# Kernel optimization log

Hardware: AMD Instinct MI355X
Metric: run time of the kernel (lower is better)

Reference implementation:

```python
import itertools
import jax, jax.numpy as jnp
import numpy as np

H, W, DIM, NH, WS = 64, 64, 384, 12, 7
HD = DIM // NH            # head dim = key_dim (attn_ratio=1)
N = WS * WS               # tokens per window
SCALE = HD ** -0.5
EPS = 1e-5
BATCH = 4
HID = int(DIM * 4.0)


def _bias_idxs():
    points = list(itertools.product(range(WS), range(WS)))
    offsets, idxs = {}, []
    for p1 in points:
        for p2 in points:
            off = (abs(p1[0] - p2[0]), abs(p1[1] - p2[1]))
            if off not in offsets:
                offsets[off] = len(offsets)
            idxs.append(offsets[off])
    return np.asarray(idxs, dtype=np.int32).reshape(N, N)

BIAS_IDXS = _bias_idxs()              # [N, N] static
NUM_OFFSETS = int(BIAS_IDXS.max()) + 1  # 49 for a 7x7 window


def setup_inputs() -> dict:
    key = jax.random.key(0)
    ks = jax.random.split(key, 10)
    rn = lambda k, shp, s=0.02: jax.random.normal(k, shp, jnp.float32) * s
    return {
        "x": jax.random.normal(ks[0], (BATCH, H * W, DIM), jnp.float32),
        "ln1_g": jnp.ones((DIM,), jnp.float32),
        "ln1_b": jnp.zeros((DIM,), jnp.float32),
        "qkv_w": rn(ks[1], (DIM, 3 * DIM)),
        "qkv_b": jnp.zeros((3 * DIM,), jnp.float32),
        "proj_w": rn(ks[2], (DIM, DIM)),
        "proj_b": jnp.zeros((DIM,), jnp.float32),
        "attn_bias": rn(ks[3], (NH, NUM_OFFSETS), 0.1),
        "conv_w": rn(ks[4], (DIM, 1, 3, 3), 0.1),  # depthwise OIHW
        "bn_g": jnp.ones((DIM,), jnp.float32),
        "bn_b": jnp.zeros((DIM,), jnp.float32),
        "bn_mean": rn(ks[5], (DIM,), 0.05),
        "bn_var": jax.random.uniform(ks[6], (DIM,), jnp.float32, 0.5, 1.5),
        "ln2_g": jnp.ones((DIM,), jnp.float32),
        "ln2_b": jnp.zeros((DIM,), jnp.float32),
        "fc1_w": rn(ks[7], (DIM, HID)),
        "fc1_b": jnp.zeros((HID,), jnp.float32),
        "fc2_w": rn(ks[8], (HID, DIM)),
        "fc2_b": jnp.zeros((DIM,), jnp.float32),
    }


def _ln(x, g, b):
    m = x.mean(-1, keepdims=True)
    v = jnp.var(x, axis=-1, keepdims=True)
    return (x - m) * jax.lax.rsqrt(v + EPS) * g + b


def reference(x, ln1_g, ln1_b, qkv_w, qkv_b, proj_w, proj_b, attn_bias,
              conv_w, bn_g, bn_b, bn_mean, bn_var, ln2_g, ln2_b,
              fc1_w, fc1_b, fc2_w, fc2_b):
    b, hw, c = x.shape
    res = x
    # --- window partition with padding ---
    pad_b = (-H) % WS
    pad_r = (-W) % WS
    pH, pW = H + pad_b, W + pad_r
    nH, nW = pH // WS, pW // WS
    xw = x.reshape(b, H, W, c)
    xw = jnp.pad(xw, ((0, 0), (0, pad_b), (0, pad_r), (0, 0)))
    xw = xw.reshape(b, nH, WS, nW, WS, c).transpose(0, 1, 3, 2, 4, 5)
    xw = xw.reshape(b * nH * nW, N, c)  # [Bw, N, C]
    # --- attention (pre-LN, relative position bias) ---
    xn = _ln(xw, ln1_g, ln1_b)
    qkv = (xn @ qkv_w + qkv_b).reshape(-1, N, NH, 3 * HD)
    q, k, v = jnp.split(qkv, [HD, 2 * HD], axis=-1)  # each [Bw, N, NH, HD]
    bias = attn_bias[:, BIAS_IDXS]                    # [NH, N, N]
    scores = jnp.einsum('bnhd,bmhd->bhnm', q, k) * SCALE + bias
    a = jax.nn.softmax(scores, axis=-1)
    o = jnp.einsum('bhnm,bmhd->bnhd', a, v).reshape(-1, N, NH * HD)
    xw = o @ proj_w + proj_b
    # --- window reverse + unpad ---
    xw = xw.reshape(b, nH, nW, WS, WS, c).transpose(0, 1, 3, 2, 4, 5)
    xw = xw.reshape(b, pH, pW, c)[:, :H, :W].reshape(b, hw, c)
    x = res + xw
    # --- depthwise 3x3 conv + BatchNorm (eval) ---
    xc = x.transpose(0, 2, 1).reshape(b, c, H, W)
    xc = jax.lax.conv_general_dilated(
        xc, conv_w, (1, 1), ((1, 1), (1, 1)),
        feature_group_count=c,
        dimension_numbers=('NCHW', 'OIHW', 'NCHW'))
    xc = (xc - bn_mean[:, None, None]) * jax.lax.rsqrt(bn_var[:, None, None] + EPS) \
         * bn_g[:, None, None] + bn_b[:, None, None]
    x = xc.reshape(b, c, hw).transpose(0, 2, 1)
    # --- MLP (pre-LN, GELU) with residual ---
    h1 = jax.nn.gelu(_ln(x, ln2_g, ln2_b) @ fc1_w + fc1_b, approximate=False)
    return x + (h1 @ fc2_w + fc2_b)
```

## Files before the change

kernel.cpp:

```cpp
#include <hip/hip_runtime.h>
#include <cstdint>


typedef __bf16 bf16x8 __attribute__((ext_vector_type(8)));
typedef __bf16 bf16x4 __attribute__((ext_vector_type(4)));
typedef float  f32x4  __attribute__((ext_vector_type(4)));

#define DIM_    384
#define QKVD    1152
#define HIDD    1536
#define NTOK    49
#define NWIN    400
#define TOKENS  16384
#define PADROW  16384
#define MQKV    16512
#define SCALE_  0.17677669529663689f
#define EPS_    1e-5f

#define B_LN1   8192
#define B_PADR  1
#define B_TQKV  108
#define B_TPROJ 36
#define B_TFC1  144
#define B_TFC2  144
#define B_CONV  14
#define B_BIAS  192
#define B_TOTAL (B_LN1 + B_PADR + B_TQKV + B_TPROJ + B_TFC1 + B_TFC2 + B_CONV + B_BIAS)

__device__ __forceinline__ void gload_lds16(const void* g, void* l) {
  __builtin_amdgcn_global_load_lds(
      (__attribute__((address_space(1))) void*)g,
      (__attribute__((address_space(3))) void*)l, 16, 0, 0);
}

__device__ __forceinline__ float gelu_fast(float v) {
  float t2 = v * (1.5957691216057308f + 0.07135481627f * v * v);
  return v * __builtin_amdgcn_rcpf(1.f + __expf(-t2));
}

__device__ __forceinline__ void tile_transpose(
    const float* __restrict__ src, __bf16* __restrict__ dst,
    int K, int N, int tile, int tilesN, __bf16 (*ld)[65]) {
  int kt = tile / tilesN, nt = tile % tilesN;
  int k0 = kt * 64, n0 = nt * 64;
  int tid = threadIdx.x;
  int a = tid & 63, b4 = tid >> 6;
  #pragma unroll
  for (int i = 0; i < 16; i++) {
    int kl = b4 + i * 4;
    ld[kl][a] = (__bf16)src[(long)(k0 + kl) * N + n0 + a];
  }
  __syncthreads();
  #pragma unroll
  for (int i = 0; i < 16; i++) {
    int nl = b4 + i * 4;
    dst[(long)(n0 + nl) * K + k0 + a] = ld[a][nl];
  }
}

__global__ __launch_bounds__(256) void prep_all(
    const float* __restrict__ x, const float* __restrict__ ln1_g,
    const float* __restrict__ ln1_b, __bf16* __restrict__ xn,
    const float* __restrict__ qkv_w,  __bf16* __restrict__ wqkv,
    const float* __restrict__ proj_w, __bf16* __restrict__ wproj,
    const float* __restrict__ fc1_w,  __bf16* __restrict__ wfc1,
    const float* __restrict__ fc2_w,  __bf16* __restrict__ wfc2,
    const float* __restrict__ conv_w, float* __restrict__ wconv,
    const float* __restrict__ attn_b, float* __restrict__ bm) {
  __shared__ __bf16 tlds[64][65];
  __shared__ float red[2][4];
  int b = blockIdx.x;
  int tid = threadIdx.x;

  if (b < B_LN1) {
    int sub = tid >> 7, tl = tid & 127;
    long t = (long)b * 2 + sub;
    const float* xr = x + t * DIM_;
    float v0 = xr[tl], v1 = xr[tl + 128], v2 = xr[tl + 256];
    float s = v0 + v1 + v2, s2 = v0 * v0 + v1 * v1 + v2 * v2;
    for (int off = 32; off; off >>= 1) { s += __shfl_down(s, off); s2 += __shfl_down(s2, off); }
    if ((tl & 63) == 0) { red[sub][tl >> 6] = s; red[sub][2 + (tl >> 6)] = s2; }
    __syncthreads();
    float S = red[sub][0] + red[sub][1], S2 = red[sub][2] + red[sub][3];
    float m  = S * (1.f / DIM_);
    float rs = rsqrtf(S2 * (1.f / DIM_) - m * m + EPS_);
    __bf16* orow = xn + t * DIM_;
    orow[tl]       = (__bf16)((v0 - m) * rs * ln1_g[tl]       + ln1_b[tl]);
    orow[tl + 128] = (__bf16)((v1 - m) * rs * ln1_g[tl + 128] + ln1_b[tl + 128]);
    orow[tl + 256] = (__bf16)((v2 - m) * rs * ln1_g[tl + 256] + ln1_b[tl + 256]);
    return;
  }
  b -= B_LN1;
  if (b < B_PADR) {
    for (int i = tid; i < DIM_; i += 256)
      xn[(long)PADROW * DIM_ + i] = (__bf16)ln1_b[i];
    return;
  }
  b -= B_PADR;
  if (b < B_TQKV)  { tile_transpose(qkv_w,  wqkv,  DIM_, QKVD, b, 18, tlds); return; }
  b -= B_TQKV;
  if (b < B_TPROJ) { tile_transpose(proj_w, wproj, DIM_, DIM_, b, 6,  tlds); return; }
  b -= B_TPROJ;
  if (b < B_TFC1)  { tile_transpose(fc1_w,  wfc1,  DIM_, HIDD, b, 24, tlds); return; }
  b -= B_TFC1;
  if (b < B_TFC2)  { tile_transpose(fc2_w,  wfc2,  HIDD, DIM_, b, 6,  tlds); return; }
  b -= B_TFC2;
  if (b < B_CONV) {
    int id = b * 256 + tid;
    if (id < 3456) {
      int ch = id / 9, k = id % 9;
      wconv[k * DIM_ + ch] = conv_w[id];
    }
    return;
  }
  b -= B_CONV;
  {
    int id = b * 256 + tid;
    int h = id >> 12, q = (id >> 6) & 63, kk = id & 63;
    float v;
    if (kk >= NTOK)      v = -1e30f;
    else if (q >= NTOK)  v = 0.f;
    else {
      int idx = abs(q / 7 - kk / 7) * 7 + abs(q % 7 - kk % 7);
      v = attn_b[h * NTOK + idx];
    }
    bm[id] = v;
  }
}

__global__ __launch_bounds__(384) void conv_bn_ln2(
    const float* __restrict__ x1, const float* __restrict__ wT,
    const float* __restrict__ bng, const float* __restrict__ bnb,
    const float* __restrict__ mean, const float* __restrict__ var,
    const float* __restrict__ g2, const float* __restrict__ b2,
    float* __restrict__ x2, __bf16* __restrict__ xln2) {
  int tid = threadIdx.x;
  int p = tid / 96, g = tid % 96;
  int pix = blockIdx.x * 4 + p;
  int bb = pix >> 12, rc = pix & 4095;
  int r = rc >> 6, c = rc & 63;
  int ch = g << 2;

  f32x4 acc = (f32x4){0.f, 0.f, 0.f, 0.f};
  #pragma unroll
  for (int dr = -1; dr <= 1; dr++) {
    int rr = r + dr;
    if (rr < 0 || rr >= 64) continue;
    #pragma unroll
    for (int dc = -1; dc <= 1; dc++) {
      int cc = c + dc;
      if (cc < 0 || cc >= 64) continue;
      f32x4 xv = *(const f32x4*)(x1 + ((long)bb * 4096 + rr * 64 + cc) * DIM_ + ch);
      f32x4 wv = *(const f32x4*)(wT + ((dr + 1) * 3 + (dc + 1)) * DIM_ + ch);
      acc += xv * wv;
    }
  }

  f32x4 gv = *(const f32x4*)(bng + ch);
  f32x4 vv = *(const f32x4*)(var + ch);
  f32x4 mv = *(const f32x4*)(mean + ch);
  f32x4 bv = *(const f32x4*)(bnb + ch);
  f32x4 y;
  #pragma unroll
  for (int j = 0; j < 4; j++) {
    float sc = gv[j] * rsqrtf(vv[j] + EPS_);
    y[j] = acc[j] * sc + (bv[j] - mv[j] * sc);
  }
  *(f32x4*)(x2 + (long)pix * DIM_ + ch) = y;

  __shared__ float pS[4][96], pS2[4][96], mS[4], rS[4];
  pS[p][g]  = y[0] + y[1] + y[2] + y[3];
  pS2[p][g] = y[0] * y[0] + y[1] * y[1] + y[2] * y[2] + y[3] * y[3];
  __syncthreads();
  if (g < 32) {
    float a  = pS[p][g]  + pS[p][g + 32]  + pS[p][g + 64];
    float a2 = pS2[p][g] + pS2[p][g + 32] + pS2[p][g + 64];
    #pragma unroll
    for (int off = 1; off < 32; off <<= 1) {
      a  += __shfl_xor(a, off);
      a2 += __shfl_xor(a2, off);
    }
    if (g == 0) {
      float m = a * (1.f / DIM_);
      mS[p] = m;
      rS[p] = rsqrtf(a2 * (1.f / DIM_) - m * m + EPS_);
    }
  }
  __syncthreads();
  float m = mS[p], rs = rS[p];
  f32x4 gg = *(const f32x4*)(g2 + ch);
  f32x4 b2v = *(const f32x4*)(b2 + ch);
  bf16x4 ov;
  #pragma unroll
  for (int j = 0; j < 4; j++) ov[j] = (__bf16)((y[j] - m) * rs * gg[j] + b2v[j]);
  *(bf16x4*)(xln2 + (long)pix * DIM_ + ch) = ov;
}

__global__ __launch_bounds__(64) void attn_mfma(const __bf16* __restrict__ qkv,
                                                const float* __restrict__ bm,
                                                __bf16* __restrict__ o) {
  int blk = blockIdx.x;
  int win = blk / 12, h = blk % 12;
  int bb = win / 100, rem = win % 100;
  int wy = rem / 10, wx = rem % 10;
  int lane = threadIdx.x;
  int quad = lane >> 4, l16 = lane & 15;

  __shared__ __align__(16) __bf16 Vt[32][72];
  __shared__ __align__(16) __bf16 P[64][72];

  const __bf16* base = qkv + h * 96;

  bf16x8 qf[4], kf[4];
  #pragma unroll
  for (int mt = 0; mt < 4; mt++) {
    int t = mt * 16 + l16;
    int ty = t / 7, tx = t % 7;
    int r = wy * 7 + ty, c = wx * 7 + tx;
    int row = (t < NTOK && r < 64 && c < 64) ? (bb * 4096 + r * 64 + c) : PADROW;
    const __bf16* rp = base + (long)row * QKVD + quad * 8;
    qf[mt] = *(const bf16x8*)(rp);
    kf[mt] = *(const bf16x8*)(rp + 32);
  }
  {
    int t = lane;
    int ty = t / 7, tx = t % 7;
    int r = wy * 7 + ty, c = wx * 7 + tx;
    int row = (t < NTOK && r < 64 && c < 64) ? (bb * 4096 + r * 64 + c) : PADROW;
    const __bf16* vp = base + (long)row * QKVD + 64;
    bf16x8 vv[4];
    #pragma unroll
    for (int i = 0; i < 4; i++) vv[i] = *(const bf16x8*)(vp + i * 8);
    #pragma unroll
    for (int i = 0; i < 4; i++)
      #pragma unroll
      for (int j = 0; j < 8; j++) Vt[i * 8 + j][lane] = vv[i][j];
  }

  f32x4 S[4][4];
  #pragma unroll
  for (int i = 0; i < 4; i++)
    #pragma unroll
    for (int j = 0; j < 4; j++) S[i][j] = (f32x4){0.f, 0.f, 0.f, 0.f};
  #pragma unroll
  for (int mt = 0; mt < 4; mt++)
    #pragma unroll
    for (int nt = 0; nt < 4; nt++)
      S[mt][nt] = __builtin_amdgcn_mfma_f32_16x16x32_bf16(qf[mt], kf[nt], S[mt][nt], 0, 0, 0);

  const float* bmh = bm + h * 4096;
  #pragma unroll
  for (int mt = 0; mt < 4; mt++)
    #pragma unroll
    for (int r = 0; r < 4; r++) {
      int q = mt * 16 + quad * 4 + r;
      #pragma unroll
      for (int nt = 0; nt < 4; nt++)
        S[mt][nt][r] = S[mt][nt][r] * SCALE_ + bmh[q * 64 + nt * 16 + l16];
    }

  #pragma unroll
  for (int mt = 0; mt < 4; mt++)
    #pragma unroll
    for (int r = 0; r < 4; r++) {
      float mx = fmaxf(fmaxf(S[mt][0][r], S[mt][1][r]), fmaxf(S[mt][2][r], S[mt][3][r]));
      #pragma unroll
      for (int off = 1; off < 16; off <<= 1) mx = fmaxf(mx, __shfl_xor(mx, off));
      float sum = 0.f;
      #pragma unroll
      for (int nt = 0; nt < 4; nt++) {
        float e = __expf(S[mt][nt][r] - mx);
        S[mt][nt][r] = e;
        sum += e;
      }
      #pragma unroll
      for (int off = 1; off < 16; off <<= 1) sum += __shfl_xor(sum, off);
      float inv = 1.f / sum;
      #pragma unroll
      for (int nt = 0; nt < 4; nt++) S[mt][nt][r] *= inv;
    }

  #pragma unroll
  for (int mt = 0; mt < 4; mt++)
    #pragma unroll
    for (int r = 0; r < 4; r++) {
      int q = mt * 16 + quad * 4 + r;
      #pragma unroll
      for (int nt = 0; nt < 4; nt++)
        P[q][nt * 16 + l16] = (__bf16)S[mt][nt][r];
    }
  __syncthreads();

  f32x4 O[4][2];
  #pragma unroll
  for (int i = 0; i < 4; i++)
    #pragma unroll
    for (int j = 0; j < 2; j++) O[i][j] = (f32x4){0.f, 0.f, 0.f, 0.f};
  #pragma unroll
  for (int kt = 0; kt < 2; kt++) {
    bf16x8 pf[4], vf[2];
    #pragma unroll
    for (int mt = 0; mt < 4; mt++)
      pf[mt] = *(const bf16x8*)(&P[mt * 16 + l16][kt * 32 + quad * 8]);
    #pragma unroll
    for (int nt = 0; nt < 2; nt++)
      vf[nt] = *(const bf16x8*)(&Vt[nt * 16 + l16][kt * 32 + quad * 8]);
    #pragma unroll
    for (int mt = 0; mt < 4; mt++)
      #pragma unroll
      for (int nt = 0; nt < 2; nt++)
        O[mt][nt] = __builtin_amdgcn_mfma_f32_16x16x32_bf16(pf[mt], vf[nt], O[mt][nt], 0, 0, 0);
  }

  #pragma unroll
  for (int mt = 0; mt < 4; mt++)
    #pragma unroll
    for (int r = 0; r < 4; r++) {
      int q = mt * 16 + quad * 4 + r;
      if (q < NTOK) {
        int ty = q / 7, tx = q % 7;
        int rr = wy * 7 + ty, cc = wx * 7 + tx;
        if (rr < 64 && cc < 64) {
          __bf16* ob = o + ((long)bb * 4096 + rr * 64 + cc) * DIM_ + h * 32;
          #pragma unroll
          for (int nt = 0; nt < 2; nt++)
            ob[nt * 16 + l16] = (__bf16)O[mt][nt][r];
        }
      }
    }
}

template <int MODE, int TN>
__global__ void __launch_bounds__(256)
gemm_bf16(const __bf16* __restrict__ A, const __bf16* __restrict__ Bt,
          const float* __restrict__ bias, int K, int N,
          float* __restrict__ outf, __bf16* __restrict__ outb,
          const float* __restrict__ res) {
  constexpr int NT = TN / 32;
  __shared__ __align__(16) __bf16 sA[128 * 32];
  __shared__ __align__(16) __bf16 sB[TN * 32];
  int tid = threadIdx.x, lane = tid & 63, wid = tid >> 6;
  int wm = wid >> 1, wn = wid & 1;
  int quad = lane >> 4, l16 = lane & 15;
  long tileM = (long)blockIdx.x * 128;
  long tileN = (long)blockIdx.y * TN;

  f32x4 acc[4][NT];
  #pragma unroll
  for (int i = 0; i < 4; i++)
    #pragma unroll
    for (int j = 0; j < NT; j++) acc[i][j] = (f32x4){0.f, 0.f, 0.f, 0.f};

  int rr = wid * 16 + (lane >> 2);
  const __bf16* gA = A  + (tileM + rr) * (long)K + ((lane & 3) << 3);
  const __bf16* gB = Bt + (tileN + rr) * (long)K + ((lane & 3) << 3);
  const long rowskip = 64 * (long)K;

  for (int k0 = 0; k0 < K; k0 += 32) {
    gload_lds16(gA + k0,           sA + (wid << 9));
    gload_lds16(gA + k0 + rowskip, sA + ((wid + 4) << 9));
    gload_lds16(gB + k0,           sB + (wid << 9));
    if (TN == 128)
      gload_lds16(gB + k0 + rowskip, sB + ((wid + 4) << 9));
    __syncthreads();
    bf16x8 af[4], bfr[NT];
    #pragma unroll
    for (int mt = 0; mt < 4; mt++)
      af[mt] = *(const bf16x8*)(sA + ((wm * 64 + mt * 16 + l16) << 5) + (quad << 3));
    #pragma unroll
    for (int nt = 0; nt < NT; nt++)
      bfr[nt] = *(const bf16x8*)(sB + ((wn * (TN / 2) + nt * 16 + l16) << 5) + (quad << 3));
    #pragma unroll
    for (int mt = 0; mt < 4; mt++)
      #pragma unroll
      for (int nt = 0; nt < NT; nt++)
        acc[mt][nt] = __builtin_amdgcn_mfma_f32_16x16x32_bf16(af[mt], bfr[nt], acc[mt][nt], 0, 0, 0);
    __syncthreads();
  }

  float bcol[NT];
  #pragma unroll
  for (int nt = 0; nt < NT; nt++) bcol[nt] = bias[tileN + wn * (TN / 2) + nt * 16 + l16];

  #pragma unroll
  for (int mt = 0; mt < 4; mt++) {
    #pragma unroll
    for (int r = 0; r < 4; r++) {
      long row = tileM + wm * 64 + mt * 16 + quad * 4 + r;
      if (MODE == 0) {
        __bf16* orow = outb + row * (long)N;
        #pragma unroll
        for (int nt = 0; nt < NT; nt++)
          orow[tileN + wn * (TN / 2) + nt * 16 + l16] = (__bf16)(acc[mt][nt][r] + bcol[nt]);
      } else if (MODE == 2) {
        __bf16* orow = outb + row * (long)N;
        #pragma unroll
        for (int nt = 0; nt < NT; nt++) {
          float v = acc[mt][nt][r] + bcol[nt];
          orow[tileN + wn * (TN / 2) + nt * 16 + l16] = (__bf16)gelu_fast(v);
        }
      } else {
        float* orow = outf + row * (long)N;
        const float* rrow = res + row * (long)N;
        #pragma unroll
        for (int nt = 0; nt < NT; nt++) {
          long col = tileN + wn * (TN / 2) + nt * 16 + l16;
          orow[col] = acc[mt][nt][r] + bcol[nt] + rrow[col];
        }
      }
    }
  }
}

template <int MODE>
__global__ void __launch_bounds__(256)
gemm_k64(const __bf16* __restrict__ A, const __bf16* __restrict__ Bt,
         const float* __restrict__ bias, int K, int N,
         float* __restrict__ outf, __bf16* __restrict__ outb,
         const float* __restrict__ res) {
  constexpr int TN = 64, NT = 2;
  __shared__ __align__(16) __bf16 sA[2][128 * 32];
  __shared__ __align__(16) __bf16 sB[2][TN * 32];
  int tid = threadIdx.x, lane = tid & 63, wid = tid >> 6;
  int wm = wid >> 1, wn = wid & 1;
  int quad = lane >> 4, l16 = lane & 15;
  long tileM = (long)blockIdx.x * 128;
  long tileN = (long)blockIdx.y * TN;

  f32x4 acc[4][NT];
  #pragma unroll
  for (int i = 0; i < 4; i++)
    #pragma unroll
    for (int j = 0; j < NT; j++) acc[i][j] = (f32x4){0.f, 0.f, 0.f, 0.f};

  int rr = wid * 16 + (lane >> 2);
  const __bf16* gA = A  + (tileM + rr) * (long)K + ((lane & 3) << 3);
  const __bf16* gB = Bt + (tileN + rr) * (long)K + ((lane & 3) << 3);
  const long rowskip = 64 * (long)K;

  for (int k0 = 0; k0 < K; k0 += 64) {
    #pragma unroll
    for (int h = 0; h < 2; h++) {
      const int ko = k0 + h * 32;
      gload_lds16(gA + ko,           &sA[h][wid << 9]);
      gload_lds16(gA + ko + rowskip, &sA[h][(wid + 4) << 9]);
      gload_lds16(gB + ko,           &sB[h][wid << 9]);
    }
    __syncthreads();
    #pragma unroll
    for (int h = 0; h < 2; h++) {
      bf16x8 af[4], bfr[NT];
      #pragma unroll
      for (int mt = 0; mt < 4; mt++)
        af[mt] = *(const bf16x8*)(&sA[h][((wm * 64 + mt * 16 + l16) << 5) + (quad << 3)]);
      #pragma unroll
      for (int nt = 0; nt < NT; nt++)
        bfr[nt] = *(const bf16x8*)(&sB[h][((wn * 32 + nt * 16 + l16) << 5) + (quad << 3)]);
      #pragma unroll
      for (int mt = 0; mt < 4; mt++)
        #pragma unroll
        for (int nt = 0; nt < NT; nt++)
          acc[mt][nt] = __builtin_amdgcn_mfma_f32_16x16x32_bf16(af[mt], bfr[nt], acc[mt][nt], 0, 0, 0);
    }
    __syncthreads();
  }

  float bcol[NT];
  #pragma unroll
  for (int nt = 0; nt < NT; nt++) bcol[nt] = bias[tileN + wn * 32 + nt * 16 + l16];

  #pragma unroll
  for (int mt = 0; mt < 4; mt++) {
    #pragma unroll
    for (int r = 0; r < 4; r++) {
      long row = tileM + wm * 64 + mt * 16 + quad * 4 + r;
      if (MODE == 2) {
        __bf16* orow = outb + row * (long)N;
        #pragma unroll
        for (int nt = 0; nt < NT; nt++) {
          float v = acc[mt][nt][r] + bcol[nt];
          orow[tileN + wn * 32 + nt * 16 + l16] = (__bf16)gelu_fast(v);
        }
      } else {
        float* orow = outf + row * (long)N;
        const float* rrow = res + row * (long)N;
        #pragma unroll
        for (int nt = 0; nt < NT; nt++) {
          long col = tileN + wn * 32 + nt * 16 + l16;
          orow[col] = acc[mt][nt][r] + bcol[nt] + rrow[col];
        }
      }
    }
  }
}

extern "C" void kernel_launch(void* const* d_in, const int* in_sizes, int n_in,
                              void* d_out, int out_size, void* d_ws, size_t ws_size,
                              hipStream_t stream) {
  const float* x       = (const float*)d_in[0];
  const float* ln1_g   = (const float*)d_in[1];
  const float* ln1_b   = (const float*)d_in[2];
  const float* qkv_w   = (const float*)d_in[3];
  const float* qkv_b   = (const float*)d_in[4];
  const float* proj_w  = (const float*)d_in[5];
  const float* proj_b  = (const float*)d_in[6];
  const float* attn_b  = (const float*)d_in[7];
  const float* conv_w  = (const float*)d_in[8];
  const float* bn_g    = (const float*)d_in[9];
  const float* bn_b    = (const float*)d_in[10];
  const float* bn_mean = (const float*)d_in[11];
  const float* bn_var  = (const float*)d_in[12];
  const float* ln2_g   = (const float*)d_in[13];
  const float* ln2_b   = (const float*)d_in[14];
  const float* fc1_w   = (const float*)d_in[15];
  const float* fc1_b   = (const float*)d_in[16];
  const float* fc2_w   = (const float*)d_in[17];
  const float* fc2_b   = (const float*)d_in[18];

  char* p = (char*)d_ws;
  __bf16* WQKV = (__bf16*)p;  p += 884736;
  __bf16* WPROJ = (__bf16*)p; p += 294912;
  __bf16* WFC1 = (__bf16*)p;  p += 1179648;
  __bf16* WFC2 = (__bf16*)p;  p += 1179648;
  float*  WCONV = (float*)p;  p += 13824;
  char* region = p;           p += 63307776;
  float* X1 = (float*)p;      p += 25165824;
  float* X2 = (float*)p;      p += 25165824;
  __bf16* XN   = (__bf16*)region;
  __bf16* QKVB = (__bf16*)(region + 12681216);
  __bf16* OBUF = (__bf16*)(region + 50724864);
  __bf16* XLN2 = (__bf16*)region;
  __bf16* H1   = (__bf16*)(region + 12681216);
  float*  BM   = X1;
  float* OUT = (float*)d_out;

  prep_all<<<B_TOTAL, 256, 0, stream>>>(x, ln1_g, ln1_b, XN,
                                        qkv_w, WQKV, proj_w, WPROJ,
                                        fc1_w, WFC1, fc2_w, WFC2,
                                        conv_w, WCONV, attn_b, BM);

  gemm_bf16<0, 128><<<dim3(MQKV / 128, QKVD / 128), 256, 0, stream>>>(
      XN, WQKV, qkv_b, DIM_, QKVD, nullptr, QKVB, nullptr);

  attn_mfma<<<NWIN * 12, 64, 0, stream>>>(QKVB, BM, OBUF);

  gemm_k64<3><<<dim3(TOKENS / 128, DIM_ / 64), 256, 0, stream>>>(
      OBUF, WPROJ, proj_b, DIM_, DIM_, X1, nullptr, x);

  conv_bn_ln2<<<TOKENS / 4, 384, 0, stream>>>(X1, WCONV, bn_g, bn_b, bn_mean, bn_var,
                                              ln2_g, ln2_b, X2, XLN2);

  gemm_k64<2><<<dim3(TOKENS / 128, HIDD / 64), 256, 0, stream>>>(
      XLN2, WFC1, fc1_b, DIM_, HIDD, nullptr, H1, nullptr);

  gemm_k64<3><<<dim3(TOKENS / 128, DIM_ / 64), 256, 0, stream>>>(
      H1, WFC2, fc2_b, HIDD, DIM_, OUT, nullptr, X2);
}
```

Measured before the change: 277.5 us.

## Swizzle GEMM LDS layout and store conv residual in bf16

The GEMM kernels now rotate each lane's global source chunk and read LDS at a matching swizzled slot, so the MFMA fragment reads from shared memory spread across banks instead of conflicting. Separately, the conv+BN output X2, used as the residual for fc2, is written and read as bf16 instead of fp32 through a new MODE 4 epilogue, which halves that tensor's memory traffic. The cost is reduced precision in the final residual add and slightly more index arithmetic per lane.

```diff
diff --git a/kernel.cpp b/kernel.cpp
--- a/kernel.cpp
+++ b/kernel.cpp
@@ -133,7 +133,7 @@
     const float* __restrict__ bng, const float* __restrict__ bnb,
     const float* __restrict__ mean, const float* __restrict__ var,
     const float* __restrict__ g2, const float* __restrict__ b2,
-    float* __restrict__ x2, __bf16* __restrict__ xln2) {
+    __bf16* __restrict__ x2, __bf16* __restrict__ xln2) {
   int tid = threadIdx.x;
   int p = tid / 96, g = tid % 96;
   int pix = blockIdx.x * 4 + p;
@@ -166,7 +166,12 @@
     float sc = gv[j] * rsqrtf(vv[j] + EPS_);
     y[j] = acc[j] * sc + (bv[j] - mv[j] * sc);
   }
-  *(f32x4*)(x2 + (long)pix * DIM_ + ch) = y;
+  {
+    bf16x4 xv2;
+    #pragma unroll
+    for (int j = 0; j < 4; j++) xv2[j] = (__bf16)y[j];
+    *(bf16x4*)(x2 + (long)pix * DIM_ + ch) = xv2;
+  }
 
   __shared__ float pS[4][96], pS2[4][96], mS[4], rS[4];
   pS[p][g]  = y[0] + y[1] + y[2] + y[3];
@@ -329,6 +334,7 @@
       }
     }
 }
+
 
 template <int MODE, int TN>
 __global__ void __launch_bounds__(256)
@@ -352,9 +358,11 @@
     for (int j = 0; j < NT; j++) acc[i][j] = (f32x4){0.f, 0.f, 0.f, 0.f};
 
   int rr = wid * 16 + (lane >> 2);
-  const __bf16* gA = A  + (tileM + rr) * (long)K + ((lane & 3) << 3);
-  const __bf16* gB = Bt + (tileN + rr) * (long)K + ((lane & 3) << 3);
+  int sc = ((lane & 3) - (lane >> 3)) & 3;
+  const __bf16* gA = A  + (tileM + rr) * (long)K + (sc << 3);
+  const __bf16* gB = Bt + (tileN + rr) * (long)K + (sc << 3);
   const long rowskip = 64 * (long)K;
+  int slot = (((l16 >> 1) + quad) & 3) << 3;
 
   for (int k0 = 0; k0 < K; k0 += 32) {
     gload_lds16(gA + k0,           sA + (wid << 9));
@@ -366,10 +374,10 @@
     bf16x8 af[4], bfr[NT];
     #pragma unroll
     for (int mt = 0; mt < 4; mt++)
-      af[mt] = *(const bf16x8*)(sA + ((wm * 64 + mt * 16 + l16) << 5) + (quad << 3));
+      af[mt] = *(const bf16x8*)(sA + ((wm * 64 + mt * 16 + l16) << 5) + slot);
     #pragma unroll
     for (int nt = 0; nt < NT; nt++)
-      bfr[nt] = *(const bf16x8*)(sB + ((wn * (TN / 2) + nt * 16 + l16) << 5) + (quad << 3));
+      bfr[nt] = *(const bf16x8*)(sB + ((wn * (TN / 2) + nt * 16 + l16) << 5) + slot);
     #pragma unroll
     for (int mt = 0; mt < 4; mt++)
       #pragma unroll
@@ -417,7 +425,7 @@
 gemm_k64(const __bf16* __restrict__ A, const __bf16* __restrict__ Bt,
          const float* __restrict__ bias, int K, int N,
          float* __restrict__ outf, __bf16* __restrict__ outb,
-         const float* __restrict__ res) {
+         const void* __restrict__ res) {
   constexpr int TN = 64, NT = 2;
   __shared__ __align__(16) __bf16 sA[2][128 * 32];
   __shared__ __align__(16) __bf16 sB[2][TN * 32];
@@ -434,9 +442,11 @@
     for (int j = 0; j < NT; j++) acc[i][j] = (f32x4){0.f, 0.f, 0.f, 0.f};
 
   int rr = wid * 16 + (lane >> 2);
-  const __bf16* gA = A  + (tileM + rr) * (long)K + ((lane & 3) << 3);
-  const __bf16* gB = Bt + (tileN + rr) * (long)K + ((lane & 3) << 3);
+  int sc = ((lane & 3) - (lane >> 3)) & 3;
+  const __bf16* gA = A  + (tileM + rr) * (long)K + (sc << 3);
+  const __bf16* gB = Bt + (tileN + rr) * (long)K + (sc << 3);
   const long rowskip = 64 * (long)K;
+  int slot = (((l16 >> 1) + quad) & 3) << 3;
 
   for (int k0 = 0; k0 < K; k0 += 64) {
     #pragma unroll
@@ -452,10 +462,10 @@
       bf16x8 af[4], bfr[NT];
       #pragma unroll
       for (int mt = 0; mt < 4; mt++)
-        af[mt] = *(const bf16x8*)(&sA[h][((wm * 64 + mt * 16 + l16) << 5) + (quad << 3)]);
+        af[mt] = *(const bf16x8*)(&sA[h][((wm * 64 + mt * 16 + l16) << 5) + slot]);
       #pragma unroll
       for (int nt = 0; nt < NT; nt++)
-        bfr[nt] = *(const bf16x8*)(&sB[h][((wn * 32 + nt * 16 + l16) << 5) + (quad << 3)]);
+        bfr[nt] = *(const bf16x8*)(&sB[h][((wn * 32 + nt * 16 + l16) << 5) + slot]);
       #pragma unroll
       for (int mt = 0; mt < 4; mt++)
         #pragma unroll
@@ -481,13 +491,21 @@
           float v = acc[mt][nt][r] + bcol[nt];
           orow[tileN + wn * 32 + nt * 16 + l16] = (__bf16)gelu_fast(v);
         }
-      } else {
+      } else if (MODE == 3) {
         float* orow = outf + row * (long)N;
-        const float* rrow = res + row * (long)N;
+        const float* rrow = (const float*)res + row * (long)N;
         #pragma unroll
         for (int nt = 0; nt < NT; nt++) {
           long col = tileN + wn * 32 + nt * 16 + l16;
           orow[col] = acc[mt][nt][r] + bcol[nt] + rrow[col];
+        }
+      } else {
+        float* orow = outf + row * (long)N;
+        const __bf16* rrow = (const __bf16*)res + row * (long)N;
+        #pragma unroll
+        for (int nt = 0; nt < NT; nt++) {
+          long col = tileN + wn * 32 + nt * 16 + l16;
+          orow[col] = acc[mt][nt][r] + bcol[nt] + (float)rrow[col];
         }
       }
     }
@@ -525,7 +543,7 @@
   float*  WCONV = (float*)p;  p += 13824;
   char* region = p;           p += 63307776;
   float* X1 = (float*)p;      p += 25165824;
-  float* X2 = (float*)p;      p += 25165824;
+  __bf16* X2 = (__bf16*)p;    p += 12582912;
   __bf16* XN   = (__bf16*)region;
   __bf16* QKVB = (__bf16*)(region + 12681216);
   __bf16* OBUF = (__bf16*)(region + 50724864);
@@ -553,6 +571,6 @@
   gemm_k64<2><<<dim3(TOKENS / 128, HIDD / 64), 256, 0, stream>>>(
       XLN2, WFC1, fc1_b, DIM_, HIDD, nullptr, H1, nullptr);
 
-  gemm_k64<3><<<dim3(TOKENS / 128, DIM_ / 64), 256, 0, stream>>>(
+  gemm_k64<4><<<dim3(TOKENS / 128, DIM_ / 64), 256, 0, stream>>>(
       H1, WFC2, fc2_b, HIDD, DIM_, OUT, nullptr, X2);
 }
```

Result: no change. 276.7 us (-0.3%).
